# Kernel optimization log

Hardware: AMD Instinct MI355X
Metric: run time of the kernel (lower is better)

The kernel has to match this reference:

```python
import jax, jax.numpy as jnp
import numpy as np

B, S, D = 2, 2048, 1024
H, HD = 16, 64  # num_attention_heads, attention_head_size


def setup_inputs() -> dict:
    key = jax.random.key(0)
    ks = jax.random.split(key, 8)
    std = 0.02
    return {
        "hidden_states": jax.random.normal(ks[0], (B, S, D), dtype=jnp.float32),
        "attention_mask": jnp.zeros((B, 1, 1, S), dtype=jnp.float32),
        "Wq": jax.random.normal(ks[1], (D, D), dtype=jnp.float32) * std,
        "bq": jnp.zeros((D,), dtype=jnp.float32),
        "Wk": jax.random.normal(ks[2], (D, D), dtype=jnp.float32) * std,
        "bk": jnp.zeros((D,), dtype=jnp.float32),
        "Wv": jax.random.normal(ks[3], (D, D), dtype=jnp.float32) * std,
        "bv": jnp.zeros((D,), dtype=jnp.float32),
    }


def reference(hidden_states, attention_mask, Wq, bq, Wk, bk, Wv, bv):
    b, s, d = hidden_states.shape

    def split_heads(x):  # [b,s,D] -> [b,H,s,HD]
        return x.reshape(b, s, H, HD).transpose(0, 2, 1, 3)

    q = split_heads(hidden_states @ Wq + bq)
    k = split_heads(hidden_states @ Wk + bk)
    v = split_heads(hidden_states @ Wv + bv)

    scores = jnp.einsum("bhqd,bhkd->bhqk", q, k) / jnp.sqrt(jnp.float32(HD))
    scores = scores + attention_mask  # additive mask, broadcast [b,1,1,s]
    probs = jax.nn.softmax(scores, axis=-1)  # dropout is identity at inference
    ctx = jnp.einsum("bhqk,bhkd->bhqd", probs, v)
    out = ctx.transpose(0, 2, 1, 3).reshape(b, s, d)
    return out
```

## Files before the change

kernel.cpp:

```cpp
#include <hip/hip_runtime.h>
#include <math.h>

#define CB 2
#define CS 2048
#define CD 1024
#define CH 16
#define CHD 64
#define CM (CB*CS)

#define QSCALE 0.18033688f
#define LOG2E  1.44269504f
#define BLOG   40.0f

typedef unsigned short u16;
using bf16x8 = __attribute__((ext_vector_type(8))) short;
using u16x8  = __attribute__((ext_vector_type(8))) unsigned short;
using f32x4  = __attribute__((ext_vector_type(4))) float;
using f32x16 = __attribute__((ext_vector_type(16))) float;
using u32x4  = __attribute__((ext_vector_type(4))) unsigned int;

__device__ __forceinline__ u16 f2bf(float f) {
    unsigned int u = __float_as_uint(f);
    u = (u + 0x7FFFu + ((u >> 16) & 1u)) >> 16;
    return (u16)u;
}

__device__ __forceinline__ unsigned cvt_pk_bf16(float lo, float hi) {
    unsigned r;
    asm("v_cvt_pk_bf16_f32 %0, %1, %2" : "=v"(r) : "v"(lo), "v"(hi));
    return r;
}

__device__ __forceinline__ void load_lds16(const u16* g, u16* l) {
    __builtin_amdgcn_global_load_lds(
        (const __attribute__((address_space(1))) unsigned int*)g,
        (__attribute__((address_space(3))) unsigned int*)l, 16, 0, 0);
}

__global__ __launch_bounds__(256)
void convert_x(const float* __restrict__ X, u16* __restrict__ Xb)
{
    size_t i = ((size_t)blockIdx.x * 256 + threadIdx.x) * 8;
    float4 v0 = *(const float4*)(X + i);
    float4 v1 = *(const float4*)(X + i + 4);
    u16x8 o;
    o[0] = f2bf(v0.x); o[1] = f2bf(v0.y); o[2] = f2bf(v0.z); o[3] = f2bf(v0.w);
    o[4] = f2bf(v1.x); o[5] = f2bf(v1.y); o[6] = f2bf(v1.z); o[7] = f2bf(v1.w);
    *(u16x8*)(Xb + i) = o;
}

__global__ __launch_bounds__(256)
void convert_wt(const float* __restrict__ Wq, const float* __restrict__ Wk,
                const float* __restrict__ Wv, u16* __restrict__ Wt)
{
    const int z = blockIdx.z;
    const float* W = (z == 0) ? Wq : (z == 1) ? Wk : Wv;
    const float sc = (z == 0) ? QSCALE : 1.0f;
    u16* Wo = Wt + (size_t)z * CD * CD;

    __shared__ u16 T[64][72];
    const int k0 = blockIdx.x << 6;
    const int n0 = blockIdx.y << 6;
    const int tid = threadIdx.x;

    #pragma unroll
    for (int it = 0; it < 4; ++it) {
        int r = (tid >> 4) + (it << 4);
        int c = (tid & 15) << 2;
        float4 v = *(const float4*)(W + (size_t)(k0 + r) * CD + n0 + c);
        T[c + 0][r] = f2bf(v.x * sc);
        T[c + 1][r] = f2bf(v.y * sc);
        T[c + 2][r] = f2bf(v.z * sc);
        T[c + 3][r] = f2bf(v.w * sc);
    }
    __syncthreads();
    #pragma unroll
    for (int it = 0; it < 2; ++it) {
        int cc = tid + (it << 8);
        int n  = cc >> 3;
        int ch = (cc & 7) << 3;
        *(uint4*)(Wo + (size_t)(n0 + n) * CD + k0 + ch) = *(const uint4*)&T[n][ch];
    }
}

__global__ __launch_bounds__(256, 3)
void qkv_gemm_mfma(const u16* __restrict__ Xb, const u16* __restrict__ Wt,
                   const float* __restrict__ bq, const float* __restrict__ bk,
                   const float* __restrict__ bv,
                   u16* __restrict__ Qb, u16* __restrict__ Kb,
                   u16* __restrict__ Vt)
{
    const int z = blockIdx.z;
    const u16* W = Wt + (size_t)z * CD * CD;
    const float* bias = (z == 0) ? bq : (z == 1) ? bk : bv;
    const float bscale = (z == 0) ? QSCALE : 1.0f;

    __shared__ u16 smem[16384];
    u16* As = smem;
    u16* Bs = smem + 8192;

    const int tid  = threadIdx.x;
    const int w    = tid >> 6;
    const int l    = tid & 63;
    const int l15  = l & 15;
    const int quad = l >> 4;
    const int wm   = w >> 1;
    const int wn   = w & 1;

    const int row0 = blockIdx.x << 7;
    const int n0   = blockIdx.y << 7;

    f32x4 acc[4][4];
    #pragma unroll
    for (int mi = 0; mi < 4; ++mi)
        #pragma unroll
        for (int nt = 0; nt < 4; ++nt)
            acc[mi][nt] = (f32x4){0.f, 0.f, 0.f, 0.f};

    const u16* Ag = Xb + (size_t)row0 * CD;
    const u16* Bg = W  + (size_t)n0   * CD;
    const int lr8 = l >> 3;
    const int ls  = l & 7;
    const int lg  = (ls ^ lr8) << 3;
    const int q7  = l15 & 7;

    for (int k0 = 0; k0 < CD; k0 += 64) {
        __syncthreads();
        #pragma unroll
        for (int i = 0; i < 4; ++i) {
            int r = w * 32 + 8 * i + lr8;
            load_lds16(Ag + (size_t)r * CD + k0 + lg, As + (size_t)(w * 32 + 8 * i) * 64);
            load_lds16(Bg + (size_t)r * CD + k0 + lg, Bs + (size_t)(w * 32 + 8 * i) * 64);
        }
        __syncthreads();

        #pragma unroll
        for (int kk = 0; kk < 2; ++kk) {
            bf16x8 af[4], bfr[4];
            #pragma unroll
            for (int mi = 0; mi < 4; ++mi)
                af[mi] = *(const bf16x8*)
                    &As[(wm * 64 + mi * 16 + l15) * 64 + (((kk * 4 + quad) ^ q7) << 3)];
            #pragma unroll
            for (int nt = 0; nt < 4; ++nt)
                bfr[nt] = *(const bf16x8*)
                    &Bs[(wn * 64 + nt * 16 + l15) * 64 + (((kk * 4 + quad) ^ q7) << 3)];
            #pragma unroll
            for (int mi = 0; mi < 4; ++mi)
                #pragma unroll
                for (int nt = 0; nt < 4; ++nt)
                    acc[mi][nt] = __builtin_amdgcn_mfma_f32_16x16x32_bf16(
                        af[mi], bfr[nt], acc[mi][nt], 0, 0, 0);
        }
    }

    __syncthreads();

    if (z < 2) {
        u16* Og = (z == 0) ? Qb : Kb;
        float bb[4];
        #pragma unroll
        for (int nt = 0; nt < 4; ++nt)
            bb[nt] = bias[n0 + wn * 64 + nt * 16 + l15] * bscale;

        u16 (*Ct)[136] = (u16(*)[136])smem;
        #pragma unroll
        for (int mh = 0; mh < 2; ++mh) {
            if (wm == mh) {
                #pragma unroll
                for (int nt = 0; nt < 4; ++nt)
                    #pragma unroll
                    for (int mi = 0; mi < 4; ++mi)
                        #pragma unroll
                        for (int r = 0; r < 4; ++r)
                            Ct[mi * 16 + quad * 4 + r][wn * 64 + nt * 16 + l15] =
                                f2bf(acc[mi][nt][r] + bb[nt]);
            }
            __syncthreads();
            #pragma unroll
            for (int it = 0; it < 4; ++it) {
                int c  = tid + (it << 8);
                int rl = c >> 4;
                int ck = c & 15;
                uint4 d = *(const uint4*)&Ct[rl][ck * 8];
                int gcol = n0 + ck * 8;
                int h = gcol >> 6, hd = gcol & 63;
                int m = row0 + mh * 64 + rl;
                int b = m >> 11, s = m & (CS - 1);
                *(uint4*)(Og + ((size_t)(b * CH + h) * CS + s) * CHD + hd) = d;
            }
            __syncthreads();
        }
    } else {
        u16 (*Ct)[136] = (u16(*)[136])smem;
        #pragma unroll
        for (int nh = 0; nh < 2; ++nh) {
            if (wn == nh) {
                #pragma unroll
                for (int nt = 0; nt < 4; ++nt) {
                    int col = n0 + nh * 64 + nt * 16 + l15;
                    float bb = bias[col];
                    #pragma unroll
                    for (int mi = 0; mi < 4; ++mi)
                        #pragma unroll
                        for (int r = 0; r < 4; ++r) {
                            int ml = wm * 64 + mi * 16 + quad * 4 + r;
                            Ct[nt * 16 + l15][ml] = f2bf(acc[mi][nt][r] + bb);
                        }
                }
            }
            __syncthreads();
            #pragma unroll
            for (int it = 0; it < 4; ++it) {
                int c   = tid + (it << 8);
                int dvl = c >> 4;
                int ch  = c & 15;
                uint4 vdat = *(const uint4*)&Ct[dvl][ch * 8];
                int col = n0 + nh * 64 + dvl;
                int h   = col >> 6;
                int dv  = col & 63;
                int m0  = row0 + ch * 8;
                int b   = m0 >> 11;
                int s0  = m0 & (CS - 1);
                *(uint4*)(Vt + (((size_t)(b * CH + h)) * CHD + dv) * CS + s0) = vdat;
            }
            __syncthreads();
        }
    }
}


#define ATTN_MLOAD(KT)                                                        \
    f32x4 mv[8];                                                              \
    _Pragma("unroll")                                                         \
    for (int st = 0; st < 2; ++st)                                            \
        _Pragma("unroll")                                                     \
        for (int g = 0; g < 4; ++g)                                           \
            mv[st * 4 + g] = *(const f32x4*)(mrh + ((KT) << 6) + st * 32 +    \
                                             g * 8 + hi * 4);

#define ATTN_STAGE(KT, KD, VD)                                                \
    {                                                                         \
        const int k0s = (KT) << 6;                                            \
        _Pragma("unroll")                                                     \
        for (int i = 0; i < 2; ++i) {                                         \
            const int rl = (qh << 4) + (i << 3);                              \
            load_lds16(Kph + (size_t)(k0s + rl + lr8) * CHD + lg, (KD) + rl * 64); \
            load_lds16(Vph + (size_t)(rl + lr8) * CS + k0s + lg,  (VD) + rl * 64); \
        }                                                                     \
    }

#define ATTN_TILE(KC, VC)                                                     \
    {                                                                         \
        _Pragma("unroll")                                                     \
        for (int st = 0; st < 2; ++st) {                                      \
            bf16x8 kf[4];                                                     \
            _Pragma("unroll")                                                 \
            for (int c = 0; c < 4; ++c)                                       \
                kf[c] = *(const bf16x8*)&(KC)[(st * 32 + l31) * 64 +          \
                            ((((c << 1) + hi) ^ sw7) << 3)];                  \
            f32x16 s;                                                         \
            _Pragma("unroll")                                                 \
            for (int g = 0; g < 4; ++g)                                       \
                _Pragma("unroll")                                             \
                for (int j = 0; j < 4; ++j)                                   \
                    s[g * 4 + j] = fmaf(mv[st * 4 + g][j], LOG2E, -BLOG);     \
            _Pragma("unroll")                                                 \
            for (int c = 0; c < 4; ++c)                                       \
                s = __builtin_amdgcn_mfma_f32_32x32x16_bf16(kf[c], qf[c], s,  \
                                                            0, 0, 0);         \
            _Pragma("unroll")                                                 \
            for (int r = 0; r < 16; ++r) s[r] = exp2f(s[r]);                  \
            lsum += ((s[0] + s[1]) + (s[2] + s[3])) +                         \
                    ((s[4] + s[5]) + (s[6] + s[7])) +                         \
                    ((s[8] + s[9]) + (s[10] + s[11])) +                       \
                    ((s[12] + s[13]) + (s[14] + s[15]));                      \
            _Pragma("unroll")                                                 \
            for (int cc = 0; cc < 2; ++cc) {                                  \
                unsigned px  = cvt_pk_bf16(s[8 * cc + 0], s[8 * cc + 1]);     \
                unsigned px2 = cvt_pk_bf16(s[8 * cc + 2], s[8 * cc + 3]);     \
                unsigned py  = cvt_pk_bf16(s[8 * cc + 4], s[8 * cc + 5]);     \
                unsigned py2 = cvt_pk_bf16(s[8 * cc + 6], s[8 * cc + 7]);     \
                unsigned t1  = __shfl_xor(hi ? px : py, 32);                  \
                unsigned t2  = __shfl_xor(hi ? px2 : py2, 32);                \
                union { u32x4 u; bf16x8 v; } pa;                              \
                pa.u[0] = hi ? t1 : px;                                       \
                pa.u[1] = hi ? t2 : px2;                                      \
                pa.u[2] = hi ? py : t1;                                       \
                pa.u[3] = hi ? py2 : t2;                                      \
                const int c = st * 2 + cc;                                    \
                bf16x8 vlo = *(const bf16x8*)&(VC)[l31 * 64 +                 \
                                 ((((c << 1) + hi) ^ sw7) << 3)];             \
                bf16x8 vhi = *(const bf16x8*)&(VC)[(32 + l31) * 64 +          \
                                 ((((c << 1) + hi) ^ sw7) << 3)];             \
                O0 = __builtin_amdgcn_mfma_f32_32x32x16_bf16(pa.v, vlo, O0,   \
                                                             0, 0, 0);        \
                O1 = __builtin_amdgcn_mfma_f32_32x32x16_bf16(pa.v, vhi, O1,   \
                                                             0, 0, 0);        \
            }                                                                 \
        }                                                                     \
    }

__global__ __launch_bounds__(512, 2)
void attn_mfma(const u16* __restrict__ Qg, const u16* __restrict__ Kg,
               const u16* __restrict__ Vtg, const float* __restrict__ mask,
               float* __restrict__ out)
{
    __shared__ u16 smem[32768];

    const int flat = blockIdx.y * 16 + blockIdx.x;
    const int nf   = ((flat & 7) << 6) + (flat >> 3);
    const int q0   = (nf & 15) << 7;
    const int bh   = nf >> 4;
    const int b    = bh >> 4;
    const int h    = bh & 15;

    const int tid = threadIdx.x;
    const int w   = tid >> 6;
    const int qh  = w & 3;
    const int kh  = w >> 2;
    const int l   = tid & 63;
    const int l31 = l & 31;
    const int hi  = l >> 5;
    const int lr8 = l >> 3;
    const int lg  = ((l & 7) ^ lr8) << 3;
    const int sw7 = l31 & 7;

    const u16* Qp    = Qg  + (size_t)bh * CS * CHD;
    const u16* Kph   = Kg  + ((size_t)bh * CS + (kh << 10)) * CHD;
    const u16* Vph   = Vtg + (size_t)bh * CHD * CS + (kh << 10);
    const float* mrh = mask + (size_t)b * CS + (kh << 10);

    u16* K0 = smem + (kh << 13);
    u16* K1 = K0 + 4096;
    u16* V0 = smem + 16384 + (kh << 13);
    u16* V1 = V0 + 4096;

    bf16x8 qf[4];
    #pragma unroll
    for (int c = 0; c < 4; ++c)
        qf[c] = *(const bf16x8*)(
            Qp + (size_t)(q0 + qh * 32 + l31) * CHD + c * 16 + hi * 8);

    f32x16 O0, O1;
    #pragma unroll
    for (int r = 0; r < 16; ++r) { O0[r] = 0.f; O1[r] = 0.f; }
    float lsum = 0.f;

    ATTN_STAGE(0, K0, V0);
    __syncthreads();

    #pragma unroll 1
    for (int kt = 0; kt < 16; kt += 2) {
        {
            ATTN_MLOAD(kt);
            __builtin_amdgcn_sched_barrier(0);
            ATTN_STAGE(kt + 1, K1, V1);
            __builtin_amdgcn_sched_barrier(0);
            ATTN_TILE(K0, V0);
            __syncthreads();
        }
        {
            ATTN_MLOAD(kt + 1);
            __builtin_amdgcn_sched_barrier(0);
            if (kt + 2 < 16) ATTN_STAGE(kt + 2, K0, V0);
            __builtin_amdgcn_sched_barrier(0);
            ATTN_TILE(K1, V1);
            __syncthreads();
        }
    }

    const float lsf = lsum + __shfl_xor(lsum, 32);

    float* ob   = (float*)smem;
    float* lbuf = (float*)(smem + 16384);

    if (kh == 1) {
        float* obw = ob + (qh << 11);
        #pragma unroll
        for (int r = 0; r < 16; ++r) {
            const int ql = (r & 3) + ((r >> 2) << 3) + (hi << 2);
            obw[ql * 64 + l31]      = O0[r];
            obw[ql * 64 + 32 + l31] = O1[r];
        }
        if (hi == 0) lbuf[(qh << 5) + l31] = lsf;
    }
    __syncthreads();

    if (kh == 0) {
        const float inv = 1.0f / (lsf + lbuf[(qh << 5) + l31]);
        const float* obw = ob + (qh << 11);
        #pragma unroll
        for (int r = 0; r < 16; ++r) {
            const int ql   = (r & 3) + ((r >> 2) << 3) + (hi << 2);
            const float iv = __shfl(inv, ql);
            float* orow = out + ((size_t)b * CS + q0 + (qh << 5) + ql) * CD + h * CHD;
            orow[l31]      = (O0[r] + obw[ql * 64 + l31]) * iv;
            orow[32 + l31] = (O1[r] + obw[ql * 64 + 32 + l31]) * iv;
        }
    }
}

extern "C" void kernel_launch(void* const* d_in, const int* in_sizes, int n_in,
                              void* d_out, int out_size, void* d_ws, size_t ws_size,
                              hipStream_t stream)
{
    const float* X    = (const float*)d_in[0];
    const float* mask = (const float*)d_in[1];
    const float* Wq   = (const float*)d_in[2];
    const float* bq   = (const float*)d_in[3];
    const float* Wk   = (const float*)d_in[4];
    const float* bk   = (const float*)d_in[5];
    const float* Wv   = (const float*)d_in[6];
    const float* bv   = (const float*)d_in[7];
    float* out = (float*)d_out;

    char* ws = (char*)d_ws;
    u16* Xb = (u16*)(ws);
    u16* Wt = (u16*)(ws + ((size_t)8  << 20));
    u16* Qb = (u16*)(ws + ((size_t)14 << 20));
    u16* Kb = (u16*)(ws + ((size_t)22 << 20));
    u16* Vt = (u16*)(ws + ((size_t)30 << 20));

    convert_x<<<CM * CD / (256 * 8), 256, 0, stream>>>(X, Xb);
    convert_wt<<<dim3(16, 16, 3), 256, 0, stream>>>(Wq, Wk, Wv, Wt);
    qkv_gemm_mfma<<<dim3(CM / 128, CD / 128, 3), 256, 0, stream>>>(
        Xb, Wt, bq, bk, bv, Qb, Kb, Vt);
    attn_mfma<<<dim3(CS / 128, CB * CH), 512, 0, stream>>>(Qb, Kb, Vt, mask, out);
}
```

Before: 194.7 us.

## Load K/V fragments directly from global into registers, drop LDS and key split

The attention kernel no longer stages K and V tiles through shared memory. Each wave now loads its MFMA K, V and mask fragments straight from global memory into registers, double-buffered across key tiles. The two-way split of keys across wave groups and the LDS reduction of partial outputs are removed, so blocks shrink from 512 to 256 threads and each wave walks all 2048 keys. This removes LDS traffic and barriers, but every wave now re-reads K/V from L2/global with less reuse, and register pressure rises from the prefetch buffers.

Measured after the change: 247.9 us. +27.4%, slower.

```diff
diff --git a/kernel.cpp b/kernel.cpp
--- a/kernel.cpp
+++ b/kernel.cpp
@@ -230,45 +230,53 @@
 }
 
 
-#define ATTN_MLOAD(KT)                                                        \
-    f32x4 mv[8];                                                              \
-    _Pragma("unroll")                                                         \
-    for (int st = 0; st < 2; ++st)                                            \
+#define ATTN_LOADK(DST, KT)                                                   \
+    {                                                                         \
+        const size_t kb_ = (size_t)(KT) << 6;                                 \
         _Pragma("unroll")                                                     \
-        for (int g = 0; g < 4; ++g)                                           \
-            mv[st * 4 + g] = *(const f32x4*)(mrh + ((KT) << 6) + st * 32 +    \
-                                             g * 8 + hi * 4);
-
-#define ATTN_STAGE(KT, KD, VD)                                                \
+        for (int st = 0; st < 2; ++st)                                        \
+            _Pragma("unroll")                                                 \
+            for (int c = 0; c < 4; ++c)                                       \
+                DST[st * 4 + c] = *(const bf16x8*)(                           \
+                    Kp + (kb_ + st * 32 + l31) * CHD + c * 16 + hi * 8);      \
+    }
+
+#define ATTN_LOADM(DST, KT)                                                   \
     {                                                                         \
-        const int k0s = (KT) << 6;                                            \
+        const int kb_ = (KT) << 6;                                            \
         _Pragma("unroll")                                                     \
-        for (int i = 0; i < 2; ++i) {                                         \
-            const int rl = (qh << 4) + (i << 3);                              \
-            load_lds16(Kph + (size_t)(k0s + rl + lr8) * CHD + lg, (KD) + rl * 64); \
-            load_lds16(Vph + (size_t)(rl + lr8) * CS + k0s + lg,  (VD) + rl * 64); \
-        }                                                                     \
-    }
-
-#define ATTN_TILE(KC, VC)                                                     \
+        for (int st = 0; st < 2; ++st)                                        \
+            _Pragma("unroll")                                                 \
+            for (int g = 0; g < 4; ++g)                                       \
+                DST[st * 4 + g] = *(const f32x4*)(                            \
+                    mr + kb_ + st * 32 + g * 8 + hi * 4);                     \
+    }
+
+#define ATTN_LOADV(DST, KT)                                                   \
+    {                                                                         \
+        const size_t kb_ = (size_t)(KT) << 6;                                 \
+        _Pragma("unroll")                                                     \
+        for (int dh = 0; dh < 2; ++dh)                                        \
+            _Pragma("unroll")                                                 \
+            for (int c = 0; c < 4; ++c)                                       \
+                DST[c * 2 + dh] = *(const bf16x8*)(                           \
+                    Vp + (size_t)(dh * 32 + l31) * CS + kb_ + c * 16 + hi * 8); \
+    }
+
+#define ATTN_TILE(KF, MV, VF)                                                 \
     {                                                                         \
         _Pragma("unroll")                                                     \
         for (int st = 0; st < 2; ++st) {                                      \
-            bf16x8 kf[4];                                                     \
-            _Pragma("unroll")                                                 \
-            for (int c = 0; c < 4; ++c)                                       \
-                kf[c] = *(const bf16x8*)&(KC)[(st * 32 + l31) * 64 +          \
-                            ((((c << 1) + hi) ^ sw7) << 3)];                  \
             f32x16 s;                                                         \
             _Pragma("unroll")                                                 \
             for (int g = 0; g < 4; ++g)                                       \
                 _Pragma("unroll")                                             \
                 for (int j = 0; j < 4; ++j)                                   \
-                    s[g * 4 + j] = fmaf(mv[st * 4 + g][j], LOG2E, -BLOG);     \
+                    s[g * 4 + j] = fmaf(MV[st * 4 + g][j], LOG2E, -BLOG);     \
             _Pragma("unroll")                                                 \
             for (int c = 0; c < 4; ++c)                                       \
-                s = __builtin_amdgcn_mfma_f32_32x32x16_bf16(kf[c], qf[c], s,  \
-                                                            0, 0, 0);         \
+                s = __builtin_amdgcn_mfma_f32_32x32x16_bf16(KF[st * 4 + c],   \
+                                                            qf[c], s, 0, 0, 0); \
             _Pragma("unroll")                                                 \
             for (int r = 0; r < 16; ++r) s[r] = exp2f(s[r]);                  \
             lsum += ((s[0] + s[1]) + (s[2] + s[3])) +                         \
@@ -289,115 +297,84 @@
                 pa.u[2] = hi ? py : t1;                                       \
                 pa.u[3] = hi ? py2 : t2;                                      \
                 const int c = st * 2 + cc;                                    \
-                bf16x8 vlo = *(const bf16x8*)&(VC)[l31 * 64 +                 \
-                                 ((((c << 1) + hi) ^ sw7) << 3)];             \
-                bf16x8 vhi = *(const bf16x8*)&(VC)[(32 + l31) * 64 +          \
-                                 ((((c << 1) + hi) ^ sw7) << 3)];             \
-                O0 = __builtin_amdgcn_mfma_f32_32x32x16_bf16(pa.v, vlo, O0,   \
-                                                             0, 0, 0);        \
-                O1 = __builtin_amdgcn_mfma_f32_32x32x16_bf16(pa.v, vhi, O1,   \
-                                                             0, 0, 0);        \
+                O0 = __builtin_amdgcn_mfma_f32_32x32x16_bf16(pa.v,            \
+                        VF[c * 2 + 0], O0, 0, 0, 0);                          \
+                O1 = __builtin_amdgcn_mfma_f32_32x32x16_bf16(pa.v,            \
+                        VF[c * 2 + 1], O1, 0, 0, 0);                          \
             }                                                                 \
         }                                                                     \
     }
 
-__global__ __launch_bounds__(512, 2)
+__global__ __launch_bounds__(256, 2)
 void attn_mfma(const u16* __restrict__ Qg, const u16* __restrict__ Kg,
                const u16* __restrict__ Vtg, const float* __restrict__ mask,
                float* __restrict__ out)
 {
-    __shared__ u16 smem[32768];
-
     const int flat = blockIdx.y * 16 + blockIdx.x;
     const int nf   = ((flat & 7) << 6) + (flat >> 3);
-    const int q0   = (nf & 15) << 7;
+    const int qb   = nf & 15;
     const int bh   = nf >> 4;
     const int b    = bh >> 4;
     const int h    = bh & 15;
 
     const int tid = threadIdx.x;
     const int w   = tid >> 6;
-    const int qh  = w & 3;
-    const int kh  = w >> 2;
     const int l   = tid & 63;
     const int l31 = l & 31;
     const int hi  = l >> 5;
-    const int lr8 = l >> 3;
-    const int lg  = ((l & 7) ^ lr8) << 3;
-    const int sw7 = l31 & 7;
-
-    const u16* Qp    = Qg  + (size_t)bh * CS * CHD;
-    const u16* Kph   = Kg  + ((size_t)bh * CS + (kh << 10)) * CHD;
-    const u16* Vph   = Vtg + (size_t)bh * CHD * CS + (kh << 10);
-    const float* mrh = mask + (size_t)b * CS + (kh << 10);
-
-    u16* K0 = smem + (kh << 13);
-    u16* K1 = K0 + 4096;
-    u16* V0 = smem + 16384 + (kh << 13);
-    u16* V1 = V0 + 4096;
+
+    const int qrow0 = (qb << 7) + (w << 5);
+    const u16* Qp  = Qg  + ((size_t)bh * CS + qrow0) * CHD;
+    const u16* Kp  = Kg  + (size_t)bh * CS * CHD;
+    const u16* Vp  = Vtg + (size_t)bh * CHD * CS;
+    const float* mr = mask + (size_t)b * CS;
 
     bf16x8 qf[4];
     #pragma unroll
     for (int c = 0; c < 4; ++c)
-        qf[c] = *(const bf16x8*)(
-            Qp + (size_t)(q0 + qh * 32 + l31) * CHD + c * 16 + hi * 8);
+        qf[c] = *(const bf16x8*)(Qp + (size_t)l31 * CHD + c * 16 + hi * 8);
 
     f32x16 O0, O1;
     #pragma unroll
     for (int r = 0; r < 16; ++r) { O0[r] = 0.f; O1[r] = 0.f; }
     float lsum = 0.f;
 
-    ATTN_STAGE(0, K0, V0);
-    __syncthreads();
+    bf16x8 kfA[8], kfB[8];
+    f32x4  mvA[8], mvB[8];
+
+    ATTN_LOADK(kfA, 0);
+    ATTN_LOADM(mvA, 0);
 
     #pragma unroll 1
-    for (int kt = 0; kt < 16; kt += 2) {
+    for (int t = 0; t < 32; t += 2) {
         {
-            ATTN_MLOAD(kt);
-            __builtin_amdgcn_sched_barrier(0);
-            ATTN_STAGE(kt + 1, K1, V1);
-            __builtin_amdgcn_sched_barrier(0);
-            ATTN_TILE(K0, V0);
-            __syncthreads();
+            bf16x8 vf[8];
+            ATTN_LOADV(vf, t);
+            ATTN_LOADK(kfB, t + 1);
+            ATTN_LOADM(mvB, t + 1);
+            ATTN_TILE(kfA, mvA, vf);
         }
         {
-            ATTN_MLOAD(kt + 1);
-            __builtin_amdgcn_sched_barrier(0);
-            if (kt + 2 < 16) ATTN_STAGE(kt + 2, K0, V0);
-            __builtin_amdgcn_sched_barrier(0);
-            ATTN_TILE(K1, V1);
-            __syncthreads();
-        }
+            bf16x8 vf[8];
+            const int tn = (t + 2) & 31;
+            ATTN_LOADV(vf, t + 1);
+            ATTN_LOADK(kfA, tn);
+            ATTN_LOADM(mvA, tn);
+            ATTN_TILE(kfB, mvB, vf);
+        }
+        if ((t & 7) == 6) __syncthreads();
     }
 
     const float lsf = lsum + __shfl_xor(lsum, 32);
-
-    float* ob   = (float*)smem;
-    float* lbuf = (float*)(smem + 16384);
-
-    if (kh == 1) {
-        float* obw = ob + (qh << 11);
-        #pragma unroll
-        for (int r = 0; r < 16; ++r) {
-            const int ql = (r & 3) + ((r >> 2) << 3) + (hi << 2);
-            obw[ql * 64 + l31]      = O0[r];
-            obw[ql * 64 + 32 + l31] = O1[r];
-        }
-        if (hi == 0) lbuf[(qh << 5) + l31] = lsf;
-    }
-    __syncthreads();
-
-    if (kh == 0) {
-        const float inv = 1.0f / (lsf + lbuf[(qh << 5) + l31]);
-        const float* obw = ob + (qh << 11);
-        #pragma unroll
-        for (int r = 0; r < 16; ++r) {
-            const int ql   = (r & 3) + ((r >> 2) << 3) + (hi << 2);
-            const float iv = __shfl(inv, ql);
-            float* orow = out + ((size_t)b * CS + q0 + (qh << 5) + ql) * CD + h * CHD;
-            orow[l31]      = (O0[r] + obw[ql * 64 + l31]) * iv;
-            orow[32 + l31] = (O1[r] + obw[ql * 64 + 32 + l31]) * iv;
-        }
+    const float inv = 1.0f / lsf;
+
+    #pragma unroll
+    for (int r = 0; r < 16; ++r) {
+        const int ql   = (r & 3) + ((r >> 2) << 3) + (hi << 2);
+        const float iv = __shfl(inv, ql);
+        float* orow = out + ((size_t)b * CS + qrow0 + ql) * CD + h * CHD;
+        orow[l31]      = O0[r] * iv;
+        orow[32 + l31] = O1[r] * iv;
     }
 }
 
@@ -426,5 +403,5 @@
     convert_wt<<<dim3(16, 16, 3), 256, 0, stream>>>(Wq, Wk, Wv, Wt);
     qkv_gemm_mfma<<<dim3(CM / 128, CD / 128, 3), 256, 0, stream>>>(
         Xb, Wt, bq, bk, bv, Qb, Kb, Vt);
-    attn_mfma<<<dim3(CS / 128, CB * CH), 512, 0, stream>>>(Qb, Kb, Vt, mask, out);
-}
+    attn_mfma<<<dim3(CS / 128, CB * CH), 256, 0, stream>>>(Qb, Kb, Vt, mask, out);
+}
```
